# Optimization experiments

Measured on AMD Instinct MI355X. Metric: run time of the kernel, lower is better.

## Reference

```python
import jax, jax.numpy as jnp
import numpy as np

N_NODES = 100000
N_EDGES = 1600000
IN_FEAT = 128
HIDDEN = 128
N_CLASSES = 40


def setup_inputs() -> dict:
    key = jax.random.key(0)
    k1, k2, k3, k4 = jax.random.split(key, 4)
    x = jax.random.normal(k1, (N_NODES, IN_FEAT), dtype=jnp.float32)
    edge_index = jax.random.randint(k2, (2, N_EDGES), 0, N_NODES, dtype=jnp.int64)
    W1 = jax.random.normal(k3, (IN_FEAT, HIDDEN), dtype=jnp.float32) * (1.0 / np.sqrt(IN_FEAT))
    b1 = jnp.zeros((HIDDEN,), dtype=jnp.float32)
    W2 = jax.random.normal(k4, (HIDDEN, N_CLASSES), dtype=jnp.float32) * (1.0 / np.sqrt(HIDDEN))
    b2 = jnp.zeros((N_CLASSES,), dtype=jnp.float32)
    return {"x": x, "edge_index": edge_index, "W1": W1, "b1": b1, "W2": W2, "b2": b2}


def _gcn_conv(x, row, col, W, b, n_nodes):
    # x: [N, F_in] -> [N, F_out]; GCNConv: lin -> gather -> deg-norm -> scatter-add -> +bias
    h = x @ W  # dense transform first (PyG GCNConv order)
    # add self-loops
    loops = jnp.arange(n_nodes, dtype=row.dtype)
    row = jnp.concatenate([row, loops])
    col = jnp.concatenate([col, loops])
    # symmetric degree normalization: deg computed on destination (col)
    deg = jax.ops.segment_sum(jnp.ones_like(col, dtype=h.dtype), col, num_segments=n_nodes)
    dis = jnp.where(deg > 0, jax.lax.rsqrt(deg), 0.0)
    norm = dis[row] * dis[col]  # [E+N]
    msg = h[row] * norm[:, None]  # [E+N, F_out] gather + scale
    out = jax.ops.segment_sum(msg, col, num_segments=n_nodes)  # scatter-add
    return out + b


def reference(x, edge_index, W1, b1, W2, b2):
    row, col = edge_index[0], edge_index[1]
    n = x.shape[0]
    h = _gcn_conv(x, row, col, W1, b1, n)
    h = jax.nn.relu(h)
    # dropout p=0 / eval mode -> identity
    h = _gcn_conv(h, row, col, W2, b2, n)
    return jax.nn.log_softmax(h, axis=1)
```

## Files before the change

kernel.cpp:

```cpp
#include <hip/hip_runtime.h>
#include <hip/hip_bf16.h>
#include <math.h>

typedef unsigned short u16x8 __attribute__((ext_vector_type(8)));
typedef short s16x8 __attribute__((ext_vector_type(8)));
typedef float f32x4 __attribute__((ext_vector_type(4)));

#define BIN_TILE 4096
#define BCAP 8192

__device__ __forceinline__ float bf2f(unsigned int u) {
    union { unsigned int i; float f; } x;
    x.i = u << 16;
    return x.f;
}
__device__ __forceinline__ unsigned short f2bf(float f) {
    __hip_bfloat16 h = __float2bfloat16(f);
    return *reinterpret_cast<unsigned short*>(&h);
}

__global__ void setup_kernel(const float* __restrict__ W1, const float* __restrict__ W2,
                             unsigned short* __restrict__ w1p, unsigned short* __restrict__ w2p,
                             unsigned* __restrict__ h2z, int* __restrict__ bcnt) {
    int bid = blockIdx.x, tid = threadIdx.x;
    if (bid < 8) {
        int t = bid * 256 + tid;
        int lane = t & 63, fc = t >> 6;
        int ct = fc >> 2, kc = fc & 3;
        int n = ct * 16 + (lane & 15);
        int k0 = kc * 32 + (lane >> 4) * 8;
        u16x8 o;
#pragma unroll
        for (int j = 0; j < 8; j++) o[j] = f2bf(W1[(size_t)(k0 + j) * 128 + n]);
        ((u16x8*)w1p)[t] = o;
    } else if (bid < 11) {
        int t = (bid - 8) * 256 + tid;
        int lane = t & 63, fc = t >> 6;
        int ct = fc >> 2, kc = fc & 3;
        int n = ct * 16 + (lane & 15);
        int k0 = kc * 32 + (lane >> 4) * 8;
        u16x8 o;
#pragma unroll
        for (int j = 0; j < 8; j++) o[j] = (n < 40) ? f2bf(W2[(size_t)(k0 + j) * 40 + n]) : (unsigned short)0;
        ((u16x8*)w2p)[t] = o;
    } else if (bid == 11) {
        if (tid < 32) h2z[tid] = 0;
    } else {
        bcnt[tid] = 0;
        bcnt[tid + 256] = 0;
    }
}

__global__ void bin_kernel(const int* __restrict__ row, const int* __restrict__ col,
                           int* __restrict__ bcnt, unsigned* __restrict__ tmp, int E, int NB) {
    __shared__ unsigned hist[512];
    int tid = threadIdx.x;
    int base = blockIdx.x * BIN_TILE;
    for (int i = tid; i < NB; i += 256) hist[i] = 0;
    __syncthreads();
#pragma unroll
    for (int i = 0; i < BIN_TILE / 256; i++) {
        int e = base + tid + i * 256;
        if (e < E) atomicAdd(&hist[col[e] >> 8], 1u);
    }
    __syncthreads();
    for (int i = tid; i < NB; i += 256) {
        unsigned h = hist[i];
        hist[i] = h ? (unsigned)atomicAdd(&bcnt[i], (int)h) : 0u;
    }
    __syncthreads();
#pragma unroll
    for (int i = 0; i < BIN_TILE / 256; i++) {
        int e = base + tid + i * 256;
        if (e < E) {
            int c = col[e], r = row[e];
            unsigned p = atomicAdd(&hist[c >> 8], 1u);
            tmp[(size_t)(c >> 8) * BCAP + p] = (unsigned)r | ((unsigned)(c & 255) << 20);
        }
    }
}

__global__ void bucket_kernel(const unsigned* __restrict__ tmp, const int* __restrict__ bcnt,
                              int* __restrict__ cnt, int* __restrict__ offs,
                              float* __restrict__ dis, int* __restrict__ csr, int N, int NB) {
    __shared__ int cntS[256], curS[256], sA[256], sB[256];
    int b = blockIdx.x;
    int tid = threadIdx.x;
    size_t tbase = (size_t)b * BCAP;

    cntS[tid] = 0;
    int partial = 0;
    if (tid < b) partial += bcnt[tid];
    if (tid + 256 < b) partial += bcnt[tid + 256];
    sA[tid] = partial;
    __syncthreads();
    for (int s = 128; s > 0; s >>= 1) {
        if (tid < s) sA[tid] += sA[tid + s];
        __syncthreads();
    }
    int start = sA[0];
    int ecnt = bcnt[b];

    for (int i = tid; i < ecnt; i += 256)
        atomicAdd(&cntS[(tmp[tbase + i] >> 20) & 255], 1);
    __syncthreads();
    int myCnt = cntS[tid];
    sA[tid] = myCnt;
    __syncthreads();
    int* src = sA;
    int* dst = sB;
    for (int off = 1; off < 256; off <<= 1) {
        dst[tid] = src[tid] + ((tid >= off) ? src[tid - off] : 0);
        __syncthreads();
        int* t = src; src = dst; dst = t;
    }
    int excl = src[tid] - myCnt;
    int node = (b << 8) + tid;
    if (node < N) {
        cnt[node] = myCnt;
        offs[node] = start + excl;
        dis[node] = rsqrtf((float)myCnt + 1.0f);
    }
    curS[tid] = excl;
    __syncthreads();
    for (int i = tid; i < ecnt; i += 256) {
        unsigned u = tmp[tbase + i];
        int cl = (u >> 20) & 255;
        int p = atomicAdd(&curS[cl], 1);
        csr[start + p] = (int)(u & 0xFFFFFu);
    }
}

__global__ void scale_cvt_kernel(const float* __restrict__ x, const float* __restrict__ dis,
                                 unsigned short* __restrict__ xbs, int N) {
    long idx = (long)blockIdx.x * blockDim.x + threadIdx.x;
    long total8 = (long)(N + 1) * 16;
    if (idx >= total8) return;
    int i = (int)(idx >> 4);
    u16x8 o;
    if (i >= N) {
#pragma unroll
        for (int k = 0; k < 8; k++) o[k] = 0;
    } else {
        float d = dis[i];
        float4 a = ((const float4*)x)[2 * idx];
        float4 b = ((const float4*)x)[2 * idx + 1];
        o[0] = f2bf(d * a.x); o[1] = f2bf(d * a.y); o[2] = f2bf(d * a.z); o[3] = f2bf(d * a.w);
        o[4] = f2bf(d * b.x); o[5] = f2bf(d * b.y); o[6] = f2bf(d * b.z); o[7] = f2bf(d * b.w);
    }
    ((u16x8*)xbs)[idx] = o;
}

__global__ void gather1_kernel(const unsigned short* __restrict__ xbs, const int* __restrict__ offs,
                               const int* __restrict__ cnt, const int* __restrict__ csr,
                               const float* __restrict__ dis, unsigned short* __restrict__ xa, int N) {
    int node = blockIdx.x * 4 + (threadIdx.x >> 6);
    int lane = threadIdx.x & 63;
    if (node >= N) return;
    int off = offs[node], dg = cnt[node];
    int g = lane >> 4, c = lane & 15;
    const u16x8* XB = (const u16x8*)xbs;
    float acc[8] = {};
    int s0 = (g      < dg) ? csr[off + g]      : N;
    int s1 = (g + 4  < dg) ? csr[off + g + 4]  : N;
    int s2 = (g + 8  < dg) ? csr[off + g + 8]  : N;
    int s3 = (g + 12 < dg) ? csr[off + g + 12] : N;
    for (int j = 0; j < dg; j += 16) {
        int jb = j + 16;
        int t0 = (jb + g      < dg) ? csr[off + jb + g]      : N;
        int t1 = (jb + g + 4  < dg) ? csr[off + jb + g + 4]  : N;
        int t2 = (jb + g + 8  < dg) ? csr[off + jb + g + 8]  : N;
        int t3 = (jb + g + 12 < dg) ? csr[off + jb + g + 12] : N;
        u16x8 v0 = XB[(size_t)s0 * 16 + c];
        u16x8 v1 = XB[(size_t)s1 * 16 + c];
        u16x8 v2 = XB[(size_t)s2 * 16 + c];
        u16x8 v3 = XB[(size_t)s3 * 16 + c];
#pragma unroll
        for (int k = 0; k < 8; k++)
            acc[k] += (bf2f(v0[k]) + bf2f(v1[k])) + (bf2f(v2[k]) + bf2f(v3[k]));
        s0 = t0; s1 = t1; s2 = t2; s3 = t3;
    }
#pragma unroll
    for (int k = 0; k < 8; k++) {
        acc[k] += __shfl_xor(acc[k], 16);
        acc[k] += __shfl_xor(acc[k], 32);
    }
    float dc = dis[node];
    u16x8 xv = XB[(size_t)node * 16 + c];
    if (lane < 16) {
        u16x8 o;
#pragma unroll
        for (int k = 0; k < 8; k++) o[k] = f2bf(dc * (acc[k] + bf2f(xv[k])));
        ((u16x8*)xa)[(size_t)node * 16 + c] = o;
    }
}

__global__ __launch_bounds__(256) void mlp_kernel(const unsigned short* __restrict__ xa,
                                                  const unsigned short* __restrict__ w1p,
                                                  const unsigned short* __restrict__ w2p,
                                                  const float* __restrict__ b1,
                                                  const float* __restrict__ dis,
                                                  unsigned short* __restrict__ h2s, int N) {
    __shared__ unsigned short a1s[64][136];
    int wv = threadIdx.x >> 6;
    int l = threadIdx.x & 63;
    int row16 = l & 15, kg = l >> 4;
    int n0 = blockIdx.x * 64;
    int rbase = n0 + wv * 16;

    f32x4 acc[8];
#pragma unroll
    for (int ct = 0; ct < 8; ct++) acc[ct] = (f32x4)0.f;
    int r = rbase + row16;
    int rc = (r < N) ? r : (N - 1);
#pragma unroll
    for (int kc = 0; kc < 4; kc++) {
        s16x8 af = *(const s16x8*)(xa + (size_t)rc * 128 + kc * 32 + kg * 8);
#pragma unroll
        for (int ct = 0; ct < 8; ct++) {
            s16x8 bf = *(const s16x8*)(w1p + (size_t)((ct * 4 + kc) * 64 + l) * 8);
            acc[ct] = __builtin_amdgcn_mfma_f32_16x16x32_bf16(af, bf, acc[ct], 0, 0, 0);
        }
    }
#pragma unroll
    for (int ct = 0; ct < 8; ct++) {
        float bb = b1[ct * 16 + row16];
#pragma unroll
        for (int v = 0; v < 4; v++)
            a1s[wv * 16 + kg * 4 + v][ct * 16 + row16] = f2bf(fmaxf(acc[ct][v] + bb, 0.f));
    }
    __syncthreads();

    f32x4 acc2[3];
#pragma unroll
    for (int ct = 0; ct < 3; ct++) acc2[ct] = (f32x4)0.f;
#pragma unroll
    for (int kc = 0; kc < 4; kc++) {
        s16x8 af = *(const s16x8*)&a1s[wv * 16 + row16][kc * 32 + kg * 8];
#pragma unroll
        for (int ct = 0; ct < 3; ct++) {
            s16x8 bf = *(const s16x8*)(w2p + (size_t)((ct * 4 + kc) * 64 + l) * 8);
            acc2[ct] = __builtin_amdgcn_mfma_f32_16x16x32_bf16(af, bf, acc2[ct], 0, 0, 0);
        }
    }
#pragma unroll
    for (int v = 0; v < 4; v++) {
        int rr = rbase + kg * 4 + v;
        if (rr < N) {
            float d = dis[rr];
#pragma unroll
            for (int ct = 0; ct < 3; ct++)
                h2s[(size_t)rr * 64 + ct * 16 + row16] = f2bf(d * acc2[ct][v]);
        }
    }
}

__global__ void gather2_kernel(const unsigned short* __restrict__ h2s, const int* __restrict__ offs,
                               const int* __restrict__ cnt, const int* __restrict__ csr,
                               const float* __restrict__ dis, const float* __restrict__ b2,
                               float* __restrict__ out, int N) {
    int node = blockIdx.x * 4 + (threadIdx.x >> 6);
    int lane = threadIdx.x & 63;
    if (node >= N) return;
    int off = offs[node], dg = cnt[node];
    int c = lane % 10;
    int g = lane / 10;
    if (g > 5) g = 5;
    const ushort4* H4 = (const ushort4*)h2s;
    float a0 = 0.f, a1 = 0.f, a2 = 0.f, a3 = 0.f;
    int s0 = (g      < dg) ? csr[off + g]      : N;
    int s1 = (g + 6  < dg) ? csr[off + g + 6]  : N;
    int s2 = (g + 12 < dg) ? csr[off + g + 12] : N;
    int s3 = (g + 18 < dg) ? csr[off + g + 18] : N;
    for (int j = 0; j < dg; j += 24) {
        int jb = j + 24;
        int t0 = (jb + g      < dg) ? csr[off + jb + g]      : N;
        int t1 = (jb + g + 6  < dg) ? csr[off + jb + g + 6]  : N;
        int t2 = (jb + g + 12 < dg) ? csr[off + jb + g + 12] : N;
        int t3 = (jb + g + 18 < dg) ? csr[off + jb + g + 18] : N;
        ushort4 u0 = H4[(size_t)s0 * 16 + c];
        ushort4 u1 = H4[(size_t)s1 * 16 + c];
        ushort4 u2 = H4[(size_t)s2 * 16 + c];
        ushort4 u3 = H4[(size_t)s3 * 16 + c];
        a0 += (bf2f(u0.x) + bf2f(u1.x)) + (bf2f(u2.x) + bf2f(u3.x));
        a1 += (bf2f(u0.y) + bf2f(u1.y)) + (bf2f(u2.y) + bf2f(u3.y));
        a2 += (bf2f(u0.z) + bf2f(u1.z)) + (bf2f(u2.z) + bf2f(u3.z));
        a3 += (bf2f(u0.w) + bf2f(u1.w)) + (bf2f(u2.w) + bf2f(u3.w));
        s0 = t0; s1 = t1; s2 = t2; s3 = t3;
    }
    float t;
    t = __shfl(a0, lane + 30); a0 += t;
    t = __shfl(a1, lane + 30); a1 += t;
    t = __shfl(a2, lane + 30); a2 += t;
    t = __shfl(a3, lane + 30); a3 += t;
    float p, q;
    p = __shfl(a0, lane + 10); q = __shfl(a0, lane + 20); a0 += p + q;
    p = __shfl(a1, lane + 10); q = __shfl(a1, lane + 20); a1 += p + q;
    p = __shfl(a2, lane + 10); q = __shfl(a2, lane + 20); a2 += p + q;
    p = __shfl(a3, lane + 10); q = __shfl(a3, lane + 20); a3 += p + q;

    bool act = lane < 10;
    float dc = dis[node];
    ushort4 uv = H4[(size_t)node * 16 + c];
    float4 bb = ((const float4*)b2)[c];
    float v0 = -INFINITY, v1 = -INFINITY, v2 = -INFINITY, v3 = -INFINITY;
    if (act) {
        v0 = dc * (a0 + bf2f(uv.x)) + bb.x;
        v1 = dc * (a1 + bf2f(uv.y)) + bb.y;
        v2 = dc * (a2 + bf2f(uv.z)) + bb.z;
        v3 = dc * (a3 + bf2f(uv.w)) + bb.w;
    }
    float m = fmaxf(fmaxf(v0, v1), fmaxf(v2, v3));
#pragma unroll
    for (int o = 32; o > 0; o >>= 1) m = fmaxf(m, __shfl_xor(m, o));
    float ex = act ? (__expf(v0 - m) + __expf(v1 - m) + __expf(v2 - m) + __expf(v3 - m)) : 0.f;
#pragma unroll
    for (int o = 32; o > 0; o >>= 1) ex += __shfl_xor(ex, o);
    float ls = __logf(ex);
    if (act) {
        float4 o4 = make_float4(v0 - m - ls, v1 - m - ls, v2 - m - ls, v3 - m - ls);
        ((float4*)(out + (size_t)node * 40))[c] = o4;
    }
}

extern "C" void kernel_launch(void* const* d_in, const int* in_sizes, int n_in,
                              void* d_out, int out_size, void* d_ws, size_t ws_size,
                              hipStream_t stream) {
    const float* x  = (const float*)d_in[0];
    const int*   ei = (const int*)d_in[1];
    const float* W1 = (const float*)d_in[2];
    const float* b1 = (const float*)d_in[3];
    const float* W2 = (const float*)d_in[4];
    const float* b2 = (const float*)d_in[5];
    float* out = (float*)d_out;

    const int N = in_sizes[0] / 128;
    const int E = in_sizes[1] / 2;
    const int* row = ei;
    const int* col = ei + E;

    const int Npad = (N + 511) & ~511;
    const int Epad = (E + 511) & ~511;
    const int NB = (N + 255) >> 8;

    int* cnt      = (int*)d_ws;
    int* offs     = cnt + Npad;
    int* bcnt     = offs + Npad;
    int* csr      = bcnt + 1024;
    unsigned* tmp = (unsigned*)(csr + Epad);
    float* dis    = (float*)(tmp + (size_t)NB * BCAP);
    unsigned short* w1p = (unsigned short*)(dis + Npad);
    unsigned short* w2p = w1p + 16384;
    unsigned short* xbs = w2p + 8192;
    unsigned short* xa  = xbs + (size_t)(N + 1) * 128;
    unsigned short* h2s = xa + (size_t)N * 128;

    setup_kernel<<<13, 256, 0, stream>>>(W1, W2, w1p, w2p,
                                         (unsigned*)(h2s + (size_t)N * 64), bcnt);
    bin_kernel<<<(E + BIN_TILE - 1) / BIN_TILE, 256, 0, stream>>>(row, col, bcnt, tmp, E, NB);
    bucket_kernel<<<NB, 256, 0, stream>>>(tmp, bcnt, cnt, offs, dis, csr, N, NB);

    {
        long total8 = (long)(N + 1) * 16;
        scale_cvt_kernel<<<(int)((total8 + 255) / 256), 256, 0, stream>>>(x, dis, xbs, N);
    }

    gather1_kernel<<<(N + 3) / 4, 256, 0, stream>>>(xbs, offs, cnt, csr, dis, xa, N);

    mlp_kernel<<<(N + 63) / 64, 256, 0, stream>>>(xa, w1p, w2p, b1, dis, h2s, N);

    gather2_kernel<<<(N + 3) / 4, 256, 0, stream>>>(h2s, offs, cnt, csr, dis, b2, out, N);
}
```

Baseline: 176.8 us.

## Fuse scale-and-convert of x into bucket kernel; cache col in registers in binning

Removes the separate scale_cvt kernel. The bucket kernel now scales each of its 256 rows of x by the per-node degree norm it just computed and writes the bf16 copy itself. The zero padding row of xbs is cleared in setup_kernel instead. Separately, bin_kernel keeps the col values from its first pass in registers so the second pass does not reload them. This saves one launch and a read of dis. The cost is that the x conversion now runs on only ~391 blocks, which may expose memory latency.

```diff
diff --git a/kernel.cpp b/kernel.cpp
--- a/kernel.cpp
+++ b/kernel.cpp
@@ -21,7 +21,8 @@
 
 __global__ void setup_kernel(const float* __restrict__ W1, const float* __restrict__ W2,
                              unsigned short* __restrict__ w1p, unsigned short* __restrict__ w2p,
-                             unsigned* __restrict__ h2z, int* __restrict__ bcnt) {
+                             unsigned* __restrict__ h2z, unsigned* __restrict__ xz,
+                             int* __restrict__ bcnt) {
     int bid = blockIdx.x, tid = threadIdx.x;
     if (bid < 8) {
         int t = bid * 256 + tid;
@@ -45,6 +46,7 @@
         ((u16x8*)w2p)[t] = o;
     } else if (bid == 11) {
         if (tid < 32) h2z[tid] = 0;
+        else if (tid < 96) xz[tid - 32] = 0;
     } else {
         bcnt[tid] = 0;
         bcnt[tid + 256] = 0;
@@ -56,12 +58,14 @@
     __shared__ unsigned hist[512];
     int tid = threadIdx.x;
     int base = blockIdx.x * BIN_TILE;
+    int cv[BIN_TILE / 256];
     for (int i = tid; i < NB; i += 256) hist[i] = 0;
     __syncthreads();
 #pragma unroll
     for (int i = 0; i < BIN_TILE / 256; i++) {
         int e = base + tid + i * 256;
-        if (e < E) atomicAdd(&hist[col[e] >> 8], 1u);
+        cv[i] = (e < E) ? col[e] : -1;
+        if (cv[i] >= 0) atomicAdd(&hist[cv[i] >> 8], 1u);
     }
     __syncthreads();
     for (int i = tid; i < NB; i += 256) {
@@ -72,8 +76,8 @@
 #pragma unroll
     for (int i = 0; i < BIN_TILE / 256; i++) {
         int e = base + tid + i * 256;
-        if (e < E) {
-            int c = col[e], r = row[e];
+        if (cv[i] >= 0) {
+            int c = cv[i], r = row[e];
             unsigned p = atomicAdd(&hist[c >> 8], 1u);
             tmp[(size_t)(c >> 8) * BCAP + p] = (unsigned)r | ((unsigned)(c & 255) << 20);
         }
@@ -82,8 +86,11 @@
 
 __global__ void bucket_kernel(const unsigned* __restrict__ tmp, const int* __restrict__ bcnt,
                               int* __restrict__ cnt, int* __restrict__ offs,
-                              float* __restrict__ dis, int* __restrict__ csr, int N, int NB) {
+                              float* __restrict__ dis, int* __restrict__ csr,
+                              const float* __restrict__ x, unsigned short* __restrict__ xbs,
+                              int N, int NB) {
     __shared__ int cntS[256], curS[256], sA[256], sB[256];
+    __shared__ float disS[256];
     int b = blockIdx.x;
     int tid = threadIdx.x;
     size_t tbase = (size_t)b * BCAP;
@@ -116,39 +123,39 @@
     }
     int excl = src[tid] - myCnt;
     int node = (b << 8) + tid;
+    float d = rsqrtf((float)myCnt + 1.0f);
     if (node < N) {
         cnt[node] = myCnt;
         offs[node] = start + excl;
-        dis[node] = rsqrtf((float)myCnt + 1.0f);
+        dis[node] = d;
     }
     curS[tid] = excl;
-    __syncthreads();
+    disS[tid] = d;
+    __syncthreads();
+
     for (int i = tid; i < ecnt; i += 256) {
         unsigned u = tmp[tbase + i];
         int cl = (u >> 20) & 255;
         int p = atomicAdd(&curS[cl], 1);
         csr[start + p] = (int)(u & 0xFFFFFu);
     }
-}
-
-__global__ void scale_cvt_kernel(const float* __restrict__ x, const float* __restrict__ dis,
-                                 unsigned short* __restrict__ xbs, int N) {
-    long idx = (long)blockIdx.x * blockDim.x + threadIdx.x;
-    long total8 = (long)(N + 1) * 16;
-    if (idx >= total8) return;
-    int i = (int)(idx >> 4);
-    u16x8 o;
-    if (i >= N) {
-#pragma unroll
-        for (int k = 0; k < 8; k++) o[k] = 0;
-    } else {
-        float d = dis[i];
-        float4 a = ((const float4*)x)[2 * idx];
-        float4 b = ((const float4*)x)[2 * idx + 1];
-        o[0] = f2bf(d * a.x); o[1] = f2bf(d * a.y); o[2] = f2bf(d * a.z); o[3] = f2bf(d * a.w);
-        o[4] = f2bf(d * b.x); o[5] = f2bf(d * b.y); o[6] = f2bf(d * b.z); o[7] = f2bf(d * b.w);
-    }
-    ((u16x8*)xbs)[idx] = o;
+
+    int rbase = b << 8;
+    const float4* X4 = (const float4*)x;
+    for (int cidx = tid; cidx < 4096; cidx += 256) {
+        int rl = cidx >> 4;
+        int ch = cidx & 15;
+        int rowg = rbase + rl;
+        if (rowg >= N) continue;
+        float dd = disS[rl];
+        long base8 = (long)rowg * 16 + ch;
+        float4 a = X4[2 * base8];
+        float4 bb = X4[2 * base8 + 1];
+        u16x8 o;
+        o[0] = f2bf(dd * a.x); o[1] = f2bf(dd * a.y); o[2] = f2bf(dd * a.z); o[3] = f2bf(dd * a.w);
+        o[4] = f2bf(dd * bb.x); o[5] = f2bf(dd * bb.y); o[6] = f2bf(dd * bb.z); o[7] = f2bf(dd * bb.w);
+        ((u16x8*)xbs)[base8] = o;
+    }
 }
 
 __global__ void gather1_kernel(const unsigned short* __restrict__ xbs, const int* __restrict__ offs,
@@ -356,14 +363,10 @@
     unsigned short* h2s = xa + (size_t)N * 128;
 
     setup_kernel<<<13, 256, 0, stream>>>(W1, W2, w1p, w2p,
-                                         (unsigned*)(h2s + (size_t)N * 64), bcnt);
+                                         (unsigned*)(h2s + (size_t)N * 64),
+                                         (unsigned*)(xbs + (size_t)N * 128), bcnt);
     bin_kernel<<<(E + BIN_TILE - 1) / BIN_TILE, 256, 0, stream>>>(row, col, bcnt, tmp, E, NB);
-    bucket_kernel<<<NB, 256, 0, stream>>>(tmp, bcnt, cnt, offs, dis, csr, N, NB);
-
-    {
-        long total8 = (long)(N + 1) * 16;
-        scale_cvt_kernel<<<(int)((total8 + 255) / 256), 256, 0, stream>>>(x, dis, xbs, N);
-    }
+    bucket_kernel<<<NB, 256, 0, stream>>>(tmp, bcnt, cnt, offs, dis, csr, x, xbs, N, NB);
 
     gather1_kernel<<<(N + 3) / 4, 256, 0, stream>>>(xbs, offs, cnt, csr, dis, xa, N);
 
```

New measurement: 175.3 us. Within noise of the previous version (-0.8%).
